# Optimization experiments

Measured on AMD Instinct MI355X. Metric: run time of the kernel, lower is better.

The kernel has to match this reference:

```python
import jax, jax.numpy as jnp
import numpy as np

N = 100000
E = 1600000
IN_C, HID, OUT_C = 500, 256, 40
K, ALPHA = 10, 0.1
LN_EPS = 1e-5


def setup_inputs() -> dict:
    key = jax.random.key(0)
    ks = jax.random.split(key, 12)
    glorot = lambda k, i, o: jax.random.normal(k, (i, o), jnp.float32) * (1.0 / np.sqrt(i))
    return {
        "x": jax.random.normal(ks[0], (N, IN_C), jnp.float32),
        "edge_index": jax.random.randint(ks[1], (2, E), 0, N, jnp.int64),
        "W1": glorot(ks[2], IN_C, HID), "b1": jnp.zeros((HID,), jnp.float32),
        "g1": jnp.ones((HID,), jnp.float32), "be1": jnp.zeros((HID,), jnp.float32),
        "W2": glorot(ks[3], HID, HID), "b2": jnp.zeros((HID,), jnp.float32),
        "g2": jnp.ones((HID,), jnp.float32), "be2": jnp.zeros((HID,), jnp.float32),
        "W3": glorot(ks[4], HID, OUT_C), "b3": jnp.zeros((OUT_C,), jnp.float32),
    }


def _layernorm(h, g, b):
    mu = jnp.mean(h, axis=-1, keepdims=True)
    var = jnp.mean(jnp.square(h - mu), axis=-1, keepdims=True)
    return (h - mu) * jax.lax.rsqrt(var + LN_EPS) * g + b


def reference(x, edge_index, W1, b1, g1, be1, W2, b2, g2, be2, W3, b3):
    # --- MLP (eval mode: dropout inactive) ---
    h = _layernorm(jax.nn.gelu(x @ W1 + b1, approximate=False), g1, be1)
    h = _layernorm(jax.nn.gelu(h @ W2 + b2, approximate=False), g2, be2)
    h = h @ W3 + b3  # [N, OUT_C]

    # --- GCN normalization with self-loops (PyG gcn_norm) ---
    loops = jnp.arange(N, dtype=edge_index.dtype)
    row = jnp.concatenate([edge_index[0], loops])  # source
    col = jnp.concatenate([edge_index[1], loops])  # target
    deg = jax.ops.segment_sum(jnp.ones_like(col, jnp.float32), col, num_segments=N)
    dinv = jnp.where(deg > 0, jax.lax.rsqrt(deg), 0.0)
    norm = dinv[row] * dinv[col]  # [E+N]

    # --- APPNP: K steps of h <- (1-alpha) * A_hat h + alpha * h0 ---
    h0 = h
    for _ in range(K):
        msg = norm[:, None] * h[row]                       # gather + scale
        agg = jax.ops.segment_sum(msg, col, num_segments=N)  # scatter-add
        h = (1.0 - ALPHA) * agg + ALPHA * h0
    return h
```

## Files before the change

### kernel.cpp

```cpp
#include <hip/hip_runtime.h>
#include <hip/hip_bf16.h>
#include <math.h>

#define N_NODES 100000
#define N_EDGES 1600000
#define IN_C    500
#define HID     256
#define OUT_C   40
#define K_ITERS 10
#define ALPHA   0.1f
#define LN_EPS  1e-5f

#define K1PAD   512
#define K2PAD   256

#define SCAN_CHUNK 1024
#define NBLK_SCAN  ((N_NODES + SCAN_CHUNK - 1) / SCAN_CHUNK)

typedef __attribute__((ext_vector_type(8))) short bf16x8;
typedef __attribute__((ext_vector_type(4))) float f32x4;

__device__ __forceinline__ void split2(float a, short& hi, short& lo) {
    const unsigned ua = __float_as_uint(a);
    hi = (short)(ua >> 16);
    const float r = a - __uint_as_float(ua & 0xffff0000u);
    lo = (short)(__float_as_uint(r) >> 16);
}

__device__ __forceinline__ void async_load16(const void* g, void* l) {
    __builtin_amdgcn_global_load_lds(
        (const __attribute__((address_space(1))) void*)g,
        (__attribute__((address_space(3))) void*)l, 16, 0, 0);
}

__global__ void deg_count_kernel(const int* __restrict__ col, int* __restrict__ cnt, int e) {
    int i = blockIdx.x * blockDim.x + threadIdx.x;
    if (i < e) atomicAdd(&cnt[col[i]], 1);
}

__global__ void dinv_kernel(const int* __restrict__ cnt, float* __restrict__ dinv, int n) {
    int i = blockIdx.x * blockDim.x + threadIdx.x;
    if (i < n) dinv[i] = rsqrtf((float)cnt[i] + 1.0f);
}

__global__ __launch_bounds__(256) void scan_partial_kernel(const int* __restrict__ cnt,
                                                           int* __restrict__ bsum) {
    __shared__ int s[256];
    const int base = blockIdx.x * SCAN_CHUNK;
    const int t = threadIdx.x;
    int sum = 0;
    #pragma unroll
    for (int j = 0; j < 4; j++) {
        int idx = base + t * 4 + j;
        if (idx < N_NODES) sum += cnt[idx];
    }
    s[t] = sum;
    __syncthreads();
    for (int off = 128; off > 0; off >>= 1) {
        if (t < off) s[t] += s[t + off];
        __syncthreads();
    }
    if (t == 0) bsum[blockIdx.x] = s[0];
}

__global__ __launch_bounds__(128) void scan_bsum_kernel(int* __restrict__ bsum, int nblk) {
    __shared__ int s[128];
    const int t = threadIdx.x;
    const int orig = (t < nblk) ? bsum[t] : 0;
    s[t] = orig;
    __syncthreads();
    for (int off = 1; off < 128; off <<= 1) {
        int v = 0;
        if (t >= off) v = s[t - off];
        __syncthreads();
        s[t] += v;
        __syncthreads();
    }
    if (t < nblk) bsum[t] = s[t] - orig;
}

__global__ __launch_bounds__(256) void scan_final_kernel(const int* __restrict__ cnt,
                                                         const int* __restrict__ bsum,
                                                         int* __restrict__ offs) {
    __shared__ int s[256];
    const int base = blockIdx.x * SCAN_CHUNK;
    const int t = threadIdx.x;
    int v[4];
    int lsum = 0;
    #pragma unroll
    for (int j = 0; j < 4; j++) {
        int idx = base + t * 4 + j;
        v[j] = (idx < N_NODES) ? cnt[idx] : 0;
        lsum += v[j];
    }
    s[t] = lsum;
    __syncthreads();
    const int orig = lsum;
    for (int off = 1; off < 256; off <<= 1) {
        int u = 0;
        if (t >= off) u = s[t - off];
        __syncthreads();
        s[t] += u;
        __syncthreads();
    }
    int run = bsum[blockIdx.x] + (s[t] - orig);
    #pragma unroll
    for (int j = 0; j < 4; j++) {
        int idx = base + t * 4 + j;
        if (idx < N_NODES) offs[idx] = run;
        run += v[j];
    }
}

__global__ void set_total_kernel(int* __restrict__ offs) {
    if (threadIdx.x == 0 && blockIdx.x == 0) offs[N_NODES] = N_EDGES;
}

__global__ void csr_fill_kernel(const int* __restrict__ row, const int* __restrict__ col,
                                const float* __restrict__ dinv, const int* __restrict__ offs,
                                int* __restrict__ cursor, int2* __restrict__ csr_ew, int e) {
    int i = blockIdx.x * blockDim.x + threadIdx.x;
    if (i >= e) return;
    const int r = row[i], c = col[i];
    const int p = offs[c] + atomicAdd(&cursor[c], 1);
    csr_ew[p] = make_int2(r, __float_as_int(dinv[r] * dinv[c]));
}

__global__ __launch_bounds__(256) void wsplit_kernel(
    const float* __restrict__ W, short* __restrict__ hi, short* __restrict__ lo,
    int K, int Nn, int Kpad)
{
    const int idx = blockIdx.x * 256 + threadIdx.x;
    if (idx >= Nn * Kpad) return;
    const int n = idx / Kpad, k = idx - n * Kpad;
    const float v = (k < K) ? W[(size_t)k * Nn + n] : 0.0f;
    short h, l;
    split2(v, h, l);
    hi[idx] = h;
    lo[idx] = l;
}

#define GBM 64
#define GBN 256
#define GBK 32
#define NSTEP1 (K1PAD / GBK)
#define NSTEP2 (K2PAD / GBK)

__global__ __launch_bounds__(256, 2) void gemm1_fused_kernel(
    const float* __restrict__ X,
    const short* __restrict__ Bhi, const short* __restrict__ Blo,
    const float* __restrict__ bias, float* __restrict__ C, int M)
{
    __shared__ short As[2][2][GBM * GBK];
    __shared__ short Bs[2][2][GBN * GBK];

    const int tid  = threadIdx.x;
    const int wid  = tid >> 6, lane = tid & 63;
    const int wm   = wid >> 1, wn = wid & 1;
    const int fm   = lane & 15, fq = lane >> 4;
    const int row0 = blockIdx.x * GBM;

    const int ar   = tid >> 2;
    const int aseg = tid & 3;
    const int gr   = min(row0 + ar, M - 1);
    const int asw  = (aseg ^ ((ar >> 1) & 3)) * 8;

    f32x4 acc[2][8] = {};

    auto stageB = [&](int ks, int buf) {
        const int k0 = ks * GBK;
        #pragma unroll
        for (int i = 0; i < 4; i++) {
            const int c  = i * 256 + tid;
            const int n  = c >> 2;
            const int k8 = ((c & 3) ^ ((n >> 1) & 3)) * 8;
            const int cb = (i * 256 + wid * 64) * 8;
            const size_t oB = (size_t)n * K1PAD + k0 + k8;
            async_load16(Bhi + oB, &Bs[buf][0][cb]);
            async_load16(Blo + oB, &Bs[buf][1][cb]);
        }
    };
    auto loadX = [&](int ks, float* v) {
        const int kb = ks * GBK + aseg * 8;
        if (kb + 8 <= IN_C) {
            const float4 v0 = *(const float4*)(X + (size_t)gr * IN_C + kb);
            const float4 v1 = *(const float4*)(X + (size_t)gr * IN_C + kb + 4);
            v[0]=v0.x; v[1]=v0.y; v[2]=v0.z; v[3]=v0.w;
            v[4]=v1.x; v[5]=v1.y; v[6]=v1.z; v[7]=v1.w;
        } else {
            #pragma unroll
            for (int j = 0; j < 8; j++)
                v[j] = (kb + j < IN_C) ? X[(size_t)gr * IN_C + kb + j] : 0.0f;
        }
    };
    auto writeA = [&](const float* v, int buf) {
        bf16x8 h8, l8;
        #pragma unroll
        for (int j = 0; j < 8; j++) { short th, tl; split2(v[j], th, tl); h8[j] = th; l8[j] = tl; }
        *(bf16x8*)&As[buf][0][ar * GBK + asw] = h8;
        *(bf16x8*)&As[buf][1][ar * GBK + asw] = l8;
    };
    auto compute = [&](int buf) {
        bf16x8 ah[2], al[2];
        #pragma unroll
        for (int tm = 0; tm < 2; tm++) {
            const int r   = wm * 32 + tm * 16 + fm;
            const int ks8 = (fq ^ ((r >> 1) & 3)) * 8;
            ah[tm] = *(const bf16x8*)&As[buf][0][r * GBK + ks8];
            al[tm] = *(const bf16x8*)&As[buf][1][r * GBK + ks8];
        }
        #pragma unroll
        for (int tn = 0; tn < 8; tn++) {
            const int cc  = wn * 128 + tn * 16 + fm;
            const int ks8 = (fq ^ ((cc >> 1) & 3)) * 8;
            const bf16x8 bh = *(const bf16x8*)&Bs[buf][0][cc * GBK + ks8];
            const bf16x8 bl = *(const bf16x8*)&Bs[buf][1][cc * GBK + ks8];
            #pragma unroll
            for (int tm = 0; tm < 2; tm++) {
                acc[tm][tn] = __builtin_amdgcn_mfma_f32_16x16x32_bf16(ah[tm], bh, acc[tm][tn], 0, 0, 0);
                acc[tm][tn] = __builtin_amdgcn_mfma_f32_16x16x32_bf16(ah[tm], bl, acc[tm][tn], 0, 0, 0);
                acc[tm][tn] = __builtin_amdgcn_mfma_f32_16x16x32_bf16(al[tm], bh, acc[tm][tn], 0, 0, 0);
            }
        }
    };

    float xvA[8], xvB[8];
    loadX(0, xvA);
    stageB(0, 0);
    loadX(1, xvB);
    writeA(xvA, 0);
    __syncthreads();

    #pragma unroll
    for (int ks = 0; ks < NSTEP1; ks += 2) {
        if (ks + 1 < NSTEP1) stageB(ks + 1, 1);
        if (ks + 2 < NSTEP1) loadX(ks + 2, xvA);
        compute(0);
        if (ks + 1 < NSTEP1) writeA(xvB, 1);
        __syncthreads();
        if (ks + 1 < NSTEP1) {
            if (ks + 2 < NSTEP1) stageB(ks + 2, 0);
            if (ks + 3 < NSTEP1) loadX(ks + 3, xvB);
            compute(1);
            if (ks + 2 < NSTEP1) writeA(xvA, 0);
            __syncthreads();
        }
    }

    #pragma unroll
    for (int tm = 0; tm < 2; tm++) {
        #pragma unroll
        for (int tn = 0; tn < 8; tn++) {
            const int gc = wn * 128 + tn * 16 + fm;
            const float bv = bias[gc];
            #pragma unroll
            for (int r = 0; r < 4; r++) {
                const int gr2 = row0 + wm * 32 + tm * 16 + fq * 4 + r;
                if (gr2 < M) {
                    float v = acc[tm][tn][r] + bv;
                    v = 0.5f * v * (1.0f + erff(v * 0.70710678118654752f));
                    C[(size_t)gr2 * 256 + gc] = v;
                }
            }
        }
    }
}

__global__ __launch_bounds__(256, 2) void gemm2_kernel(
    const short* __restrict__ Ahi, const short* __restrict__ Alo,
    const short* __restrict__ Bhi, const short* __restrict__ Blo,
    const float* __restrict__ bias, float* __restrict__ C, int M)
{
    __shared__ short As[2][2][GBM * GBK];
    __shared__ short Bs[2][2][GBN * GBK];

    const int tid  = threadIdx.x;
    const int wid  = tid >> 6, lane = tid & 63;
    const int wm   = wid >> 1, wn = wid & 1;
    const int fm   = lane & 15, fq = lane >> 4;
    const int row0 = blockIdx.x * GBM;

    f32x4 acc[2][8] = {};

    auto stage = [&](int ks, int buf) {
        const int k0 = ks * GBK;
        {
            const int m  = tid >> 2;
            const int k8 = ((tid & 3) ^ ((m >> 1) & 3)) * 8;
            const int cb = (wid * 64) * 8;
            const size_t oA = (size_t)min(row0 + m, M - 1) * K2PAD + k0 + k8;
            async_load16(Ahi + oA, &As[buf][0][cb]);
            async_load16(Alo + oA, &As[buf][1][cb]);
        }
        #pragma unroll
        for (int i = 0; i < 4; i++) {
            const int c  = i * 256 + tid;
            const int n  = c >> 2;
            const int k8 = ((c & 3) ^ ((n >> 1) & 3)) * 8;
            const int cb = (i * 256 + wid * 64) * 8;
            const size_t oB = (size_t)n * K2PAD + k0 + k8;
            async_load16(Bhi + oB, &Bs[buf][0][cb]);
            async_load16(Blo + oB, &Bs[buf][1][cb]);
        }
    };
    auto compute = [&](int buf) {
        bf16x8 ah[2], al[2];
        #pragma unroll
        for (int tm = 0; tm < 2; tm++) {
            const int r   = wm * 32 + tm * 16 + fm;
            const int ks8 = (fq ^ ((r >> 1) & 3)) * 8;
            ah[tm] = *(const bf16x8*)&As[buf][0][r * GBK + ks8];
            al[tm] = *(const bf16x8*)&As[buf][1][r * GBK + ks8];
        }
        #pragma unroll
        for (int tn = 0; tn < 8; tn++) {
            const int cc  = wn * 128 + tn * 16 + fm;
            const int ks8 = (fq ^ ((cc >> 1) & 3)) * 8;
            const bf16x8 bh = *(const bf16x8*)&Bs[buf][0][cc * GBK + ks8];
            const bf16x8 bl = *(const bf16x8*)&Bs[buf][1][cc * GBK + ks8];
            #pragma unroll
            for (int tm = 0; tm < 2; tm++) {
                acc[tm][tn] = __builtin_amdgcn_mfma_f32_16x16x32_bf16(ah[tm], bh, acc[tm][tn], 0, 0, 0);
                acc[tm][tn] = __builtin_amdgcn_mfma_f32_16x16x32_bf16(ah[tm], bl, acc[tm][tn], 0, 0, 0);
                acc[tm][tn] = __builtin_amdgcn_mfma_f32_16x16x32_bf16(al[tm], bh, acc[tm][tn], 0, 0, 0);
            }
        }
    };

    stage(0, 0);
    __syncthreads();

    #pragma unroll
    for (int ks = 0; ks < NSTEP2; ks += 2) {
        if (ks + 1 < NSTEP2) stage(ks + 1, 1);
        compute(0);
        __syncthreads();
        if (ks + 1 < NSTEP2) {
            if (ks + 2 < NSTEP2) stage(ks + 2, 0);
            compute(1);
            __syncthreads();
        }
    }

    #pragma unroll
    for (int tm = 0; tm < 2; tm++) {
        #pragma unroll
        for (int tn = 0; tn < 8; tn++) {
            const int gc = wn * 128 + tn * 16 + fm;
            const float bv = bias[gc];
            #pragma unroll
            for (int r = 0; r < 4; r++) {
                const int gr2 = row0 + wm * 32 + tm * 16 + fq * 4 + r;
                if (gr2 < M) {
                    float v = acc[tm][tn][r] + bv;
                    v = 0.5f * v * (1.0f + erff(v * 0.70710678118654752f));
                    C[(size_t)gr2 * 256 + gc] = v;
                }
            }
        }
    }
}

__global__ __launch_bounds__(256) void layernorm_split_kernel(
    const float* __restrict__ h, const float* __restrict__ g, const float* __restrict__ b,
    short* __restrict__ hi, short* __restrict__ lo, int nrows)
{
    const int wave = threadIdx.x >> 6;
    const int lane = threadIdx.x & 63;
    const int row  = blockIdx.x * 4 + wave;
    if (row >= nrows) return;

    const float* p = h + (size_t)row * HID;
    float v[4];
    float s = 0.0f;
    #pragma unroll
    for (int j = 0; j < 4; j++) { v[j] = p[lane + 64 * j]; s += v[j]; }
    #pragma unroll
    for (int off = 32; off > 0; off >>= 1) s += __shfl_xor(s, off);
    const float mu = s * (1.0f / 256.0f);

    float vs = 0.0f;
    #pragma unroll
    for (int j = 0; j < 4; j++) { float d = v[j] - mu; vs += d * d; }
    #pragma unroll
    for (int off = 32; off > 0; off >>= 1) vs += __shfl_xor(vs, off);
    const float rs = rsqrtf(vs * (1.0f / 256.0f) + LN_EPS);

    #pragma unroll
    for (int j = 0; j < 4; j++) {
        const int c = lane + 64 * j;
        const float o = (v[j] - mu) * rs * g[c] + b[c];
        short th, tl;
        split2(o, th, tl);
        hi[(size_t)row * HID + c] = th;
        lo[(size_t)row * HID + c] = tl;
    }
}

__global__ __launch_bounds__(256) void ln_gemm3_kernel(
    const float* __restrict__ h, const float* __restrict__ g, const float* __restrict__ b,
    const float* __restrict__ W, const float* __restrict__ bias,
    float* __restrict__ C, int nrows)
{
    __shared__ float Ws[HID * OUT_C];
    __shared__ float bs[OUT_C];
    __shared__ float rowbuf[4][HID];

    for (int i = threadIdx.x; i < HID * OUT_C; i += 256) Ws[i] = W[i];
    if (threadIdx.x < OUT_C) bs[threadIdx.x] = bias[threadIdx.x];

    const int wave = threadIdx.x >> 6;
    const int lane = threadIdx.x & 63;
    const int row  = blockIdx.x * 4 + wave;
    const bool alive = (row < nrows);

    if (alive) {
        const float* p = h + (size_t)row * HID;
        float v[4];
        float s = 0.0f;
        #pragma unroll
        for (int j = 0; j < 4; j++) { v[j] = p[lane + 64 * j]; s += v[j]; }
        #pragma unroll
        for (int off = 32; off > 0; off >>= 1) s += __shfl_xor(s, off);
        const float mu = s * (1.0f / 256.0f);

        float vs = 0.0f;
        #pragma unroll
        for (int j = 0; j < 4; j++) { float d = v[j] - mu; vs += d * d; }
        #pragma unroll
        for (int off = 32; off > 0; off >>= 1) vs += __shfl_xor(vs, off);
        const float rs = rsqrtf(vs * (1.0f / 256.0f) + LN_EPS);

        #pragma unroll
        for (int j = 0; j < 4; j++) {
            const int c = lane + 64 * j;
            rowbuf[wave][c] = (v[j] - mu) * rs * g[c] + b[c];
        }
    }
    __syncthreads();

    if (alive && lane < OUT_C) {
        float s = 0.0f;
        #pragma unroll 8
        for (int k = 0; k < HID; k++)
            s += rowbuf[wave][k] * Ws[k * OUT_C + lane];
        C[(size_t)row * OUT_C + lane] = s + bs[lane];
    }
}

__global__ __launch_bounds__(256) void appnp_kernel(
    const int* __restrict__ offs, const int2* __restrict__ csr_ew,
    const float* __restrict__ dinv,
    const float* __restrict__ h, const float* __restrict__ h0,
    float* __restrict__ out)
{
    const int node = blockIdx.x * 4 + (threadIdx.x >> 6);
    if (node >= N_NODES) return;
    const int lane = threadIdx.x & 63;
    const int g = lane / 10;
    const int q = lane - g * 10;
    const bool act = (lane < 60);

    const int start = offs[node];
    const int end   = offs[node + 1];

    const float d = dinv[node];
    float4 hs = make_float4(0.f, 0.f, 0.f, 0.f);
    float4 h0v = make_float4(0.f, 0.f, 0.f, 0.f);
    const size_t eidx = (size_t)node * OUT_C + (lane < 10 ? lane : 0) * 4;
    if (lane < 10) {
        hs  = *(const float4*)(h + eidx);
        h0v = *(const float4*)(h0 + eidx);
    }

    float ax = 0.0f, ay = 0.0f, az = 0.0f, aw = 0.0f;
    for (int e0 = start; e0 < end; e0 += 18) {
        const int ee0 = e0 + g, ee1 = ee0 + 6, ee2 = ee0 + 12;
        const bool a0 = act && (ee0 < end);
        const bool a1 = act && (ee1 < end);
        const bool a2 = act && (ee2 < end);
        const int2 ed0 = csr_ew[a0 ? ee0 : start];
        const int2 ed1 = csr_ew[a1 ? ee1 : start];
        const int2 ed2 = csr_ew[a2 ? ee2 : start];
        const float4 v0 = *(const float4*)(h + (size_t)ed0.x * OUT_C + q * 4);
        const float4 v1 = *(const float4*)(h + (size_t)ed1.x * OUT_C + q * 4);
        const float4 v2 = *(const float4*)(h + (size_t)ed2.x * OUT_C + q * 4);
        const float w0 = a0 ? __int_as_float(ed0.y) : 0.0f;
        const float w1 = a1 ? __int_as_float(ed1.y) : 0.0f;
        const float w2 = a2 ? __int_as_float(ed2.y) : 0.0f;
        ax += w0 * v0.x + w1 * v1.x + w2 * v2.x;
        ay += w0 * v0.y + w1 * v1.y + w2 * v2.y;
        az += w0 * v0.z + w1 * v1.z + w2 * v2.z;
        aw += w0 * v0.w + w1 * v1.w + w2 * v2.w;
    }

    ax += __shfl(ax, lane + 30); ay += __shfl(ay, lane + 30);
    az += __shfl(az, lane + 30); aw += __shfl(aw, lane + 30);
    {
        const float bx = __shfl(ax, lane + 10), cx = __shfl(ax, lane + 20);
        const float by = __shfl(ay, lane + 10), cy = __shfl(ay, lane + 20);
        const float bz = __shfl(az, lane + 10), cz = __shfl(az, lane + 20);
        const float bw = __shfl(aw, lane + 10), cw = __shfl(aw, lane + 20);
        ax += bx + cx; ay += by + cy; az += bz + cz; aw += bw + cw;
    }

    if (lane < 10) {
        const float self = d * d;
        float4 o;
        o.x = (1.0f - ALPHA) * (ax + self * hs.x) + ALPHA * h0v.x;
        o.y = (1.0f - ALPHA) * (ay + self * hs.y) + ALPHA * h0v.y;
        o.z = (1.0f - ALPHA) * (az + self * hs.z) + ALPHA * h0v.z;
        o.w = (1.0f - ALPHA) * (aw + self * hs.w) + ALPHA * h0v.w;
        *(float4*)(out + eidx) = o;
    }
}

extern "C" void kernel_launch(void* const* d_in, const int* in_sizes, int n_in,
                              void* d_out, int out_size, void* d_ws, size_t ws_size,
                              hipStream_t stream) {
    const float* x   = (const float*)d_in[0];
    const int*   ei  = (const int*)d_in[1];
    const float* W1  = (const float*)d_in[2];
    const float* b1  = (const float*)d_in[3];
    const float* g1  = (const float*)d_in[4];
    const float* be1 = (const float*)d_in[5];
    const float* W2  = (const float*)d_in[6];
    const float* b2  = (const float*)d_in[7];
    const float* g2  = (const float*)d_in[8];
    const float* be2 = (const float*)d_in[9];
    const float* W3  = (const float*)d_in[10];
    const float* b3  = (const float*)d_in[11];
    float* out = (float*)d_out;

    const int* e_row = ei;
    const int* e_col = ei + N_EDGES;

    float* ws = (float*)d_ws;
    size_t off = 0;
    float* dinv = ws + off; off += N_NODES;
    int*   cnt  = (int*)(ws + off); off += N_NODES;
    int*   offs = (int*)(ws + off); off += N_NODES + 1;
    int*   bsum = (int*)(ws + off); off += 128 + 3;
    short* W1hi = (short*)(ws + off); off += 65536;
    short* W1lo = (short*)(ws + off); off += 65536;
    short* W2hi = (short*)(ws + off); off += 32768;
    short* W2lo = (short*)(ws + off); off += 32768;
    float* t1 = ws + off; off += (size_t)N_NODES * HID;
    float* t2 = t1;
    float* regA = ws + off; off += (size_t)N_NODES * HID;
    short* A2hi = (short*)regA;
    short* A2lo = A2hi + (size_t)N_NODES * HID;
    int2*  csr_ew = (int2*)regA;
    float* h0 = regA + 2 * (size_t)N_EDGES;
    float* hA = h0 + (size_t)N_NODES * OUT_C;
    float* hB = hA + (size_t)N_NODES * OUT_C;

    hipMemsetAsync(cnt, 0, N_NODES * sizeof(int), stream);
    deg_count_kernel<<<(N_EDGES + 255) / 256, 256, 0, stream>>>(e_col, cnt, N_EDGES);
    dinv_kernel<<<(N_NODES + 255) / 256, 256, 0, stream>>>(cnt, dinv, N_NODES);
    scan_partial_kernel<<<NBLK_SCAN, 256, 0, stream>>>(cnt, bsum);
    scan_bsum_kernel<<<1, 128, 0, stream>>>(bsum, NBLK_SCAN);
    scan_final_kernel<<<NBLK_SCAN, 256, 0, stream>>>(cnt, bsum, offs);
    set_total_kernel<<<1, 64, 0, stream>>>(offs);

    wsplit_kernel<<<(256 * K1PAD + 255) / 256, 256, 0, stream>>>(W1, W1hi, W1lo, IN_C, 256, K1PAD);
    wsplit_kernel<<<(256 * K2PAD + 255) / 256, 256, 0, stream>>>(W2, W2hi, W2lo, HID, 256, K2PAD);

    {
        const int nblk = (N_NODES + GBM - 1) / GBM;
        gemm1_fused_kernel<<<nblk, 256, 0, stream>>>(x, W1hi, W1lo, b1, t1, N_NODES);
        layernorm_split_kernel<<<(N_NODES + 3) / 4, 256, 0, stream>>>(t1, g1, be1, A2hi, A2lo, N_NODES);
        gemm2_kernel<<<nblk, 256, 0, stream>>>(A2hi, A2lo, W2hi, W2lo, b2, t2, N_NODES);
        ln_gemm3_kernel<<<(N_NODES + 3) / 4, 256, 0, stream>>>(t2, g2, be2, W3, b3, h0, N_NODES);
    }

    hipMemsetAsync(cnt, 0, N_NODES * sizeof(int), stream);
    csr_fill_kernel<<<(N_EDGES + 255) / 256, 256, 0, stream>>>(
        e_row, e_col, dinv, offs, cnt, csr_ew, N_EDGES);

    const float* hcur = h0;
    for (int it = 0; it < K_ITERS; it++) {
        float* tgt = (it == K_ITERS - 1) ? out : ((it & 1) ? hB : hA);
        appnp_kernel<<<(N_NODES + 3) / 4, 256, 0, stream>>>(
            offs, csr_ew, dinv, hcur, h0, tgt);
        hcur = tgt;
    }
}
```

Before: 1.552 ms.

## Drop LDS staging in GEMMs and load MFMA fragments directly from global

Both MLP GEMM kernels stop staging A and B tiles through double-buffered shared memory with async global-to-LDS loads. Each lane now loads its bf16x8 fragments straight from global memory (splitting X to hi/lo on the fly in gemm1), and the barriers go away. The launch-bounds occupancy hint rises from 2 to 4 blocks. This removes LDS traffic and synchronisation, but it loses data reuse across waves and software pipelining, so more global/L2 traffic is likely.

```diff
diff --git a/kernel.cpp b/kernel.cpp
--- a/kernel.cpp
+++ b/kernel.cpp
@@ -25,12 +25,6 @@
     hi = (short)(ua >> 16);
     const float r = a - __uint_as_float(ua & 0xffff0000u);
     lo = (short)(__float_as_uint(r) >> 16);
-}
-
-__device__ __forceinline__ void async_load16(const void* g, void* l) {
-    __builtin_amdgcn_global_load_lds(
-        (const __attribute__((address_space(1))) void*)g,
-        (__attribute__((address_space(3))) void*)l, 16, 0, 0);
 }
 
 __global__ void deg_count_kernel(const int* __restrict__ col, int* __restrict__ cnt, int e) {
@@ -146,104 +140,60 @@
 #define NSTEP1 (K1PAD / GBK)
 #define NSTEP2 (K2PAD / GBK)
 
-__global__ __launch_bounds__(256, 2) void gemm1_fused_kernel(
+__global__ __launch_bounds__(256, 4) void gemm1_fused_kernel(
     const float* __restrict__ X,
     const short* __restrict__ Bhi, const short* __restrict__ Blo,
     const float* __restrict__ bias, float* __restrict__ C, int M)
 {
-    __shared__ short As[2][2][GBM * GBK];
-    __shared__ short Bs[2][2][GBN * GBK];
-
     const int tid  = threadIdx.x;
     const int wid  = tid >> 6, lane = tid & 63;
     const int wm   = wid >> 1, wn = wid & 1;
     const int fm   = lane & 15, fq = lane >> 4;
     const int row0 = blockIdx.x * GBM;
 
-    const int ar   = tid >> 2;
-    const int aseg = tid & 3;
-    const int gr   = min(row0 + ar, M - 1);
-    const int asw  = (aseg ^ ((ar >> 1) & 3)) * 8;
+    const float* xp0 = X + (size_t)min(row0 + wm * 32 + fm,      M - 1) * IN_C;
+    const float* xp1 = X + (size_t)min(row0 + wm * 32 + 16 + fm, M - 1) * IN_C;
 
     f32x4 acc[2][8] = {};
 
-    auto stageB = [&](int ks, int buf) {
-        const int k0 = ks * GBK;
-        #pragma unroll
-        for (int i = 0; i < 4; i++) {
-            const int c  = i * 256 + tid;
-            const int n  = c >> 2;
-            const int k8 = ((c & 3) ^ ((n >> 1) & 3)) * 8;
-            const int cb = (i * 256 + wid * 64) * 8;
-            const size_t oB = (size_t)n * K1PAD + k0 + k8;
-            async_load16(Bhi + oB, &Bs[buf][0][cb]);
-            async_load16(Blo + oB, &Bs[buf][1][cb]);
+    for (int ks = 0; ks < NSTEP1; ks++) {
+        const int kk = ks * GBK + fq * 8;
+
+        bf16x8 ah[2], al[2];
+        {
+            const float* xs[2] = { xp0, xp1 };
+            #pragma unroll
+            for (int tm = 0; tm < 2; tm++) {
+                float v[8];
+                if (kk + 8 <= IN_C) {
+                    const float4 v0 = *(const float4*)(xs[tm] + kk);
+                    const float4 v1 = *(const float4*)(xs[tm] + kk + 4);
+                    v[0]=v0.x; v[1]=v0.y; v[2]=v0.z; v[3]=v0.w;
+                    v[4]=v1.x; v[5]=v1.y; v[6]=v1.z; v[7]=v1.w;
+                } else {
+                    #pragma unroll
+                    for (int j = 0; j < 8; j++)
+                        v[j] = (kk + j < IN_C) ? xs[tm][kk + j] : 0.0f;
+                }
+                #pragma unroll
+                for (int j = 0; j < 8; j++) {
+                    short th, tl; split2(v[j], th, tl);
+                    ah[tm][j] = th; al[tm][j] = tl;
+                }
+            }
         }
-    };
-    auto loadX = [&](int ks, float* v) {
-        const int kb = ks * GBK + aseg * 8;
-        if (kb + 8 <= IN_C) {
-            const float4 v0 = *(const float4*)(X + (size_t)gr * IN_C + kb);
-            const float4 v1 = *(const float4*)(X + (size_t)gr * IN_C + kb + 4);
-            v[0]=v0.x; v[1]=v0.y; v[2]=v0.z; v[3]=v0.w;
-            v[4]=v1.x; v[5]=v1.y; v[6]=v1.z; v[7]=v1.w;
-        } else {
-            #pragma unroll
-            for (int j = 0; j < 8; j++)
-                v[j] = (kb + j < IN_C) ? X[(size_t)gr * IN_C + kb + j] : 0.0f;
-        }
-    };
-    auto writeA = [&](const float* v, int buf) {
-        bf16x8 h8, l8;
-        #pragma unroll
-        for (int j = 0; j < 8; j++) { short th, tl; split2(v[j], th, tl); h8[j] = th; l8[j] = tl; }
-        *(bf16x8*)&As[buf][0][ar * GBK + asw] = h8;
-        *(bf16x8*)&As[buf][1][ar * GBK + asw] = l8;
-    };
-    auto compute = [&](int buf) {
-        bf16x8 ah[2], al[2];
-        #pragma unroll
-        for (int tm = 0; tm < 2; tm++) {
-            const int r   = wm * 32 + tm * 16 + fm;
-            const int ks8 = (fq ^ ((r >> 1) & 3)) * 8;
-            ah[tm] = *(const bf16x8*)&As[buf][0][r * GBK + ks8];
-            al[tm] = *(const bf16x8*)&As[buf][1][r * GBK + ks8];
-        }
+
         #pragma unroll
         for (int tn = 0; tn < 8; tn++) {
-            const int cc  = wn * 128 + tn * 16 + fm;
-            const int ks8 = (fq ^ ((cc >> 1) & 3)) * 8;
-            const bf16x8 bh = *(const bf16x8*)&Bs[buf][0][cc * GBK + ks8];
-            const bf16x8 bl = *(const bf16x8*)&Bs[buf][1][cc * GBK + ks8];
+            const int cc = wn * 128 + tn * 16 + fm;
+            const bf16x8 bh = *(const bf16x8*)(Bhi + (size_t)cc * K1PAD + kk);
+            const bf16x8 bl = *(const bf16x8*)(Blo + (size_t)cc * K1PAD + kk);
             #pragma unroll
             for (int tm = 0; tm < 2; tm++) {
                 acc[tm][tn] = __builtin_amdgcn_mfma_f32_16x16x32_bf16(ah[tm], bh, acc[tm][tn], 0, 0, 0);
                 acc[tm][tn] = __builtin_amdgcn_mfma_f32_16x16x32_bf16(ah[tm], bl, acc[tm][tn], 0, 0, 0);
                 acc[tm][tn] = __builtin_amdgcn_mfma_f32_16x16x32_bf16(al[tm], bh, acc[tm][tn], 0, 0, 0);
             }
-        }
-    };
-
-    float xvA[8], xvB[8];
-    loadX(0, xvA);
-    stageB(0, 0);
-    loadX(1, xvB);
-    writeA(xvA, 0);
-    __syncthreads();
-
-    #pragma unroll
-    for (int ks = 0; ks < NSTEP1; ks += 2) {
-        if (ks + 1 < NSTEP1) stageB(ks + 1, 1);
-        if (ks + 2 < NSTEP1) loadX(ks + 2, xvA);
-        compute(0);
-        if (ks + 1 < NSTEP1) writeA(xvB, 1);
-        __syncthreads();
-        if (ks + 1 < NSTEP1) {
-            if (ks + 2 < NSTEP1) stageB(ks + 2, 0);
-            if (ks + 3 < NSTEP1) loadX(ks + 3, xvB);
-            compute(1);
-            if (ks + 2 < NSTEP1) writeA(xvA, 0);
-            __syncthreads();
         }
     }
 
@@ -266,79 +216,42 @@
     }
 }
 
-__global__ __launch_bounds__(256, 2) void gemm2_kernel(
+__global__ __launch_bounds__(256, 4) void gemm2_kernel(
     const short* __restrict__ Ahi, const short* __restrict__ Alo,
     const short* __restrict__ Bhi, const short* __restrict__ Blo,
     const float* __restrict__ bias, float* __restrict__ C, int M)
 {
-    __shared__ short As[2][2][GBM * GBK];
-    __shared__ short Bs[2][2][GBN * GBK];
-
     const int tid  = threadIdx.x;
     const int wid  = tid >> 6, lane = tid & 63;
     const int wm   = wid >> 1, wn = wid & 1;
     const int fm   = lane & 15, fq = lane >> 4;
     const int row0 = blockIdx.x * GBM;
 
+    const size_t r0 = (size_t)min(row0 + wm * 32 + fm,      M - 1) * K2PAD;
+    const size_t r1 = (size_t)min(row0 + wm * 32 + 16 + fm, M - 1) * K2PAD;
+
     f32x4 acc[2][8] = {};
 
-    auto stage = [&](int ks, int buf) {
-        const int k0 = ks * GBK;
-        {
-            const int m  = tid >> 2;
-            const int k8 = ((tid & 3) ^ ((m >> 1) & 3)) * 8;
-            const int cb = (wid * 64) * 8;
-            const size_t oA = (size_t)min(row0 + m, M - 1) * K2PAD + k0 + k8;
-            async_load16(Ahi + oA, &As[buf][0][cb]);
-            async_load16(Alo + oA, &As[buf][1][cb]);
-        }
-        #pragma unroll
-        for (int i = 0; i < 4; i++) {
-            const int c  = i * 256 + tid;
-            const int n  = c >> 2;
-            const int k8 = ((c & 3) ^ ((n >> 1) & 3)) * 8;
-            const int cb = (i * 256 + wid * 64) * 8;
-            const size_t oB = (size_t)n * K2PAD + k0 + k8;
-            async_load16(Bhi + oB, &Bs[buf][0][cb]);
-            async_load16(Blo + oB, &Bs[buf][1][cb]);
-        }
-    };
-    auto compute = [&](int buf) {
+    for (int ks = 0; ks < NSTEP2; ks++) {
+        const int kk = ks * GBK + fq * 8;
+
         bf16x8 ah[2], al[2];
-        #pragma unroll
-        for (int tm = 0; tm < 2; tm++) {
-            const int r   = wm * 32 + tm * 16 + fm;
-            const int ks8 = (fq ^ ((r >> 1) & 3)) * 8;
-            ah[tm] = *(const bf16x8*)&As[buf][0][r * GBK + ks8];
-            al[tm] = *(const bf16x8*)&As[buf][1][r * GBK + ks8];
-        }
+        ah[0] = *(const bf16x8*)(Ahi + r0 + kk);
+        al[0] = *(const bf16x8*)(Alo + r0 + kk);
+        ah[1] = *(const bf16x8*)(Ahi + r1 + kk);
+        al[1] = *(const bf16x8*)(Alo + r1 + kk);
+
         #pragma unroll
         for (int tn = 0; tn < 8; tn++) {
-            const int cc  = wn * 128 + tn * 16 + fm;
-            const int ks8 = (fq ^ ((cc >> 1) & 3)) * 8;
-            const bf16x8 bh = *(const bf16x8*)&Bs[buf][0][cc * GBK + ks8];
-            const bf16x8 bl = *(const bf16x8*)&Bs[buf][1][cc * GBK + ks8];
+            const int cc = wn * 128 + tn * 16 + fm;
+            const bf16x8 bh = *(const bf16x8*)(Bhi + (size_t)cc * K2PAD + kk);
+            const bf16x8 bl = *(const bf16x8*)(Blo + (size_t)cc * K2PAD + kk);
             #pragma unroll
             for (int tm = 0; tm < 2; tm++) {
                 acc[tm][tn] = __builtin_amdgcn_mfma_f32_16x16x32_bf16(ah[tm], bh, acc[tm][tn], 0, 0, 0);
                 acc[tm][tn] = __builtin_amdgcn_mfma_f32_16x16x32_bf16(ah[tm], bl, acc[tm][tn], 0, 0, 0);
                 acc[tm][tn] = __builtin_amdgcn_mfma_f32_16x16x32_bf16(al[tm], bh, acc[tm][tn], 0, 0, 0);
             }
-        }
-    };
-
-    stage(0, 0);
-    __syncthreads();
-
-    #pragma unroll
-    for (int ks = 0; ks < NSTEP2; ks += 2) {
-        if (ks + 1 < NSTEP2) stage(ks + 1, 1);
-        compute(0);
-        __syncthreads();
-        if (ks + 1 < NSTEP2) {
-            if (ks + 2 < NSTEP2) stage(ks + 2, 0);
-            compute(1);
-            __syncthreads();
         }
     }
 
@@ -465,7 +378,7 @@
     const int end   = offs[node + 1];
 
     const float d = dinv[node];
-    float4 hs = make_float4(0.f, 0.f, 0.f, 0.f);
+    float4 hs  = make_float4(0.f, 0.f, 0.f, 0.f);
     float4 h0v = make_float4(0.f, 0.f, 0.f, 0.f);
     const size_t eidx = (size_t)node * OUT_C + (lane < 10 ? lane : 0) * 4;
     if (lane < 10) {
```

Result: slower. 1.851 ms (+19.3%).
